# Kernel tuning notes

Measured on AMD Instinct MI355X. Metric: run time of the kernel, lower is better.

Reference implementation:

```python
import jax, jax.numpy as jnp
import numpy as np

RESO = 64
PAD = 0.1
SCALE = 8.0
PLANES = {'xz': (0, 2), 'xy': (0, 1), 'yz': (1, 2)}
PLANE_ORDER = ['xz', 'xy', 'yz']


def normalize_coordinate(p, plane):
    i, j = PLANES[plane]
    xy = jnp.stack([p[..., i], p[..., j]], axis=-1)
    xy = xy / (1.0 + PAD + 1e-3) + 0.5
    return jnp.clip(xy, 0.0, 1.0 - 1e-5)


def coordinate2index(xy, reso):
    x = (xy * reso).astype(jnp.int32)
    return x[..., 0] + reso * x[..., 1]  # (B, T)


def resblock(x, W0, b0, W1, b1, Ws):
    # ResnetBlockFC: fc_1(relu(fc_0(relu(x)))) + shortcut(x)
    net = jnp.maximum(x, 0.0) @ W0 + b0
    dx = jnp.maximum(net, 0.0) @ W1 + b1
    return x @ Ws + dx


def scatter_max_pool(c, idx_flat, num_seg):
    # c: (B, T, h); idx_flat: (B*T,) batch-offset plane indices
    B, T, h = c.shape
    pooled = jax.ops.segment_max(c.reshape(B * T, h), idx_flat, num_segments=num_seg)
    return pooled[idx_flat].reshape(B, T, h)


def plane_feature(p, c, plane):
    # scatter_mean of c into (B, c_dim, RESO, RESO); empty cells -> 0
    B, T, cd = c.shape
    R2 = RESO * RESO
    idx = coordinate2index(normalize_coordinate(p / SCALE, plane), RESO)
    idxf = (idx + jnp.arange(B, dtype=jnp.int32)[:, None] * R2).reshape(-1)
    sums = jax.ops.segment_sum(c.reshape(B * T, cd), idxf, num_segments=B * R2)
    cnt = jax.ops.segment_sum(jnp.ones((B * T,), c.dtype), idxf, num_segments=B * R2)
    mean = sums / jnp.maximum(cnt, 1.0)[:, None]
    return mean.reshape(B, R2, cd).transpose(0, 2, 1).reshape(B, cd, RESO, RESO)


def forward(p, fc_pos_W, fc_pos_b, blocks_W0, blocks_b0, blocks_W1, blocks_b1, blocks_Ws, fc_c_W, fc_c_b):
    B, T, _ = p.shape
    R2 = RESO * RESO
    offs = jnp.arange(B, dtype=jnp.int32)[:, None] * R2
    idx = {k: (coordinate2index(normalize_coordinate(p / SCALE, k), RESO) + offs).reshape(-1)
           for k in PLANE_ORDER}

    net = p @ fc_pos_W + fc_pos_b  # (B, T, 3h)
    net = resblock(net, blocks_W0[0], blocks_b0[0], blocks_W1[0], blocks_b1[0], blocks_Ws[0])
    n_blocks = blocks_W0.shape[0]
    for i in range(1, n_blocks):
        pooled = sum(scatter_max_pool(net, idx[k], B * R2) for k in PLANE_ORDER)
        meanp = jnp.broadcast_to(net.mean(axis=1, keepdims=True), net.shape)
        net = jnp.concatenate([net, pooled, meanp], axis=-1)  # (B, T, 3h)
        net = resblock(net, blocks_W0[i], blocks_b0[i], blocks_W1[i], blocks_b1[i], blocks_Ws[i])

    c = net @ fc_c_W + fc_c_b  # (B, T, c_dim)
    fea = jnp.stack([plane_feature(p, c, k) for k in PLANE_ORDER], axis=0)
    return fea  # (3, B, c_dim, RESO, RESO) in order xz, xy, yz


def setup_inputs() -> dict:
    key = jax.random.key(0)
    ks = jax.random.split(key, 10)
    B, T, dim = 16, 8192, 3
    h, c_dim, nb = 128, 128, 5
    s = 0.05
    return {
        'p': jax.random.normal(ks[0], (B, T, dim), jnp.float32) * 2.0,
        'fc_pos_W': jax.random.normal(ks[1], (dim, 3 * h), jnp.float32) * s,
        'fc_pos_b': jnp.zeros((3 * h,), jnp.float32),
        'blocks_W0': jax.random.normal(ks[2], (nb, 3 * h, h), jnp.float32) * s,
        'blocks_b0': jnp.zeros((nb, h), jnp.float32),
        'blocks_W1': jax.random.normal(ks[3], (nb, h, h), jnp.float32) * s,
        'blocks_b1': jnp.zeros((nb, h), jnp.float32),
        'blocks_Ws': jax.random.normal(ks[4], (nb, 3 * h, h), jnp.float32) * s,
        'fc_c_W': jax.random.normal(ks[5], (h, c_dim), jnp.float32) * s,
        'fc_c_b': jnp.zeros((c_dim,), jnp.float32),
    }


def reference(p, fc_pos_W, fc_pos_b, blocks_W0, blocks_b0, blocks_W1, blocks_b1, blocks_Ws, fc_c_W, fc_c_b):
    return forward(p, fc_pos_W, fc_pos_b, blocks_W0, blocks_b0, blocks_W1, blocks_b1, blocks_Ws, fc_c_W, fc_c_b)
```

## Files before the change

### kernel.cpp

```cpp
#include <hip/hip_runtime.h>

#define BT (16 * 8192)
#define NB 5
#define NCELL 65536
typedef unsigned int uint;
typedef unsigned short ushort;
typedef __attribute__((ext_vector_type(8))) short bf16x8;
typedef __attribute__((ext_vector_type(4))) float f32x4;


__device__ __forceinline__ uint f2bf(float x) {
    uint u = __float_as_uint(x);
    return (u + 0x7fffu + ((u >> 16) & 1u)) >> 16;
}
__device__ __forceinline__ float bf2f_lo(uint u) { return __uint_as_float(u << 16); }
__device__ __forceinline__ float bf2f_hi(uint u) { return __uint_as_float(u & 0xffff0000u); }
__device__ __forceinline__ uint pack2(float a, float b) { return f2bf(a) | (f2bf(b) << 16); }

__device__ __forceinline__ uint relu2(uint u) {
    uint m = (u >> 15) & 0x00010001u;
    return u & ~(m * 0xffffu);
}
__device__ __forceinline__ bf16x8 relu8(bf16x8 a) {
    uint4 u = *(uint4*)&a;
    u.x = relu2(u.x); u.y = relu2(u.y); u.z = relu2(u.z); u.w = relu2(u.w);
    return *(bf16x8*)&u;
}
__device__ __forceinline__ f32x4 bcast4(float x) { return (f32x4){x, x, x, x}; }
__device__ __forceinline__ f32x4 mfma16(bf16x8 a, bf16x8 b, f32x4 c) {
    return __builtin_amdgcn_mfma_f32_16x16x32_bf16(a, b, c, 0, 0, 0);
}

__global__ void k_idx(const float* __restrict__ p, int* __restrict__ idx) {
    int r = blockIdx.x * 256 + threadIdx.x;
    if (r >= BT) return;
    float p0 = p[3 * r + 0], p1 = p[3 * r + 1], p2 = p[3 * r + 2];
    const float DEN = (float)(1.0 + 0.1 + 1e-3);
    const float HI  = (float)(1.0 - 1e-5);
    int b = r >> 13;
    float x0 = fminf(fmaxf((p0 / 8.0f) / DEN + 0.5f, 0.0f), HI);
    float x1 = fminf(fmaxf((p1 / 8.0f) / DEN + 0.5f, 0.0f), HI);
    float x2 = fminf(fmaxf((p2 / 8.0f) / DEN + 0.5f, 0.0f), HI);
    int i0 = (int)(x0 * 64.0f);
    int i1 = (int)(x1 * 64.0f);
    int i2 = (int)(x2 * 64.0f);
    int base = b << 12;
    idx[r]          = base + i0 + (i2 << 6);
    idx[BT + r]     = base + i0 + (i1 << 6);
    idx[2 * BT + r] = base + i1 + (i2 << 6);
}

__global__ void k_hist(const int* __restrict__ idx, int* __restrict__ cnt) {
    int r = blockIdx.x * 256 + threadIdx.x;
    if (r >= BT) return;
    atomicAdd(cnt + idx[r], 1);
    atomicAdd(cnt + NCELL + idx[BT + r], 1);
    atomicAdd(cnt + 2 * NCELL + idx[2 * BT + r], 1);
}

__global__ __launch_bounds__(1024) void k_scan(const int* __restrict__ cnt,
                                               int* __restrict__ starts,
                                               int* __restrict__ cursor) {
    __shared__ int sc[1024];
    int pl = blockIdx.x, t = threadIdx.x;
    const int* c = cnt + pl * NCELL;
    int base = t * 64;
    int s = 0;
    for (int i = 0; i < 64; ++i) s += c[base + i];
    sc[t] = s;
    __syncthreads();
    for (int off = 1; off < 1024; off <<= 1) {
        int v = (t >= off) ? sc[t - off] : 0;
        __syncthreads();
        sc[t] += v;
        __syncthreads();
    }
    int run = sc[t] - s;
    for (int i = 0; i < 64; ++i) {
        int cell = base + i;
        starts[pl * NCELL + cell] = run;
        cursor[pl * NCELL + cell] = run;
        run += c[cell];
    }
}

__global__ void k_scatter_order(const int* __restrict__ idx, int* __restrict__ cursor,
                                int* __restrict__ order) {
    int r = blockIdx.x * 256 + threadIdx.x;
    if (r >= BT) return;
    for (int pl = 0; pl < 3; ++pl) {
        int cell = idx[pl * BT + r];
        int pos = atomicAdd(cursor + pl * NCELL + cell, 1);
        order[pl * BT + pos] = r;
    }
}

__global__ void k_wconv(const float* __restrict__ W0, const float* __restrict__ W1,
                        const float* __restrict__ Ws, const float* __restrict__ Wc,
                        ushort* __restrict__ wb) {
    int mat = blockIdx.y;
    int K = (mat < 5 || (mat >= 10 && mat < 15)) ? 384 : 128;
    int e = blockIdx.x * 256 + threadIdx.x;
    if (e >= K * 128) return;
    const float* src;
    size_t doff;
    if (mat < 5)       { src = W0 + (size_t)mat * 49152;        doff = (size_t)mat * 49152; }
    else if (mat < 10) { src = W1 + (size_t)(mat - 5) * 16384;  doff = 245760 + (size_t)(mat - 5) * 16384; }
    else if (mat < 15) { src = Ws + (size_t)(mat - 10) * 49152; doff = 327680 + (size_t)(mat - 10) * 49152; }
    else               { src = Wc;                              doff = 573440; }
    int ko = e & 31, n = (e >> 5) & 127, kt = e >> 12;
    wb[doff + e] = (ushort)f2bf(src[(size_t)(kt * 32 + ko) * 128 + n]);
}

__global__ __launch_bounds__(256) void k_segmax(const uint* __restrict__ netu,
                                                const int* __restrict__ starts,
                                                const int* __restrict__ cnt,
                                                const int* __restrict__ order,
                                                uint* __restrict__ segu) {
    int g = blockIdx.x * 4 + (threadIdx.x >> 6);
    int l = threadIdx.x & 63;
    int n = cnt[g];
    if (n == 0) return;
    int pl = g >> 16;
    const int* ord = order + pl * BT + starts[g];
    float m0 = -INFINITY, m1 = -INFINITY;
    int i = 0;
    for (; i + 4 <= n; i += 4) {
        uint a = netu[(size_t)ord[i] * 64 + l];
        uint b = netu[(size_t)ord[i + 1] * 64 + l];
        uint c = netu[(size_t)ord[i + 2] * 64 + l];
        uint d = netu[(size_t)ord[i + 3] * 64 + l];
        m0 = fmaxf(fmaxf(m0, fmaxf(bf2f_lo(a), bf2f_lo(b))), fmaxf(bf2f_lo(c), bf2f_lo(d)));
        m1 = fmaxf(fmaxf(m1, fmaxf(bf2f_hi(a), bf2f_hi(b))), fmaxf(bf2f_hi(c), bf2f_hi(d)));
    }
    for (; i < n; ++i) {
        uint a = netu[(size_t)ord[i] * 64 + l];
        m0 = fmaxf(m0, bf2f_lo(a));
        m1 = fmaxf(m1, bf2f_hi(a));
    }
    segu[(size_t)g * 64 + l] = pack2(m0, m1);
}

template <int MODE>
__global__ __launch_bounds__(512, 4) void k_resblock(
    const float* __restrict__ p, const uint* __restrict__ netu,
    const int* __restrict__ idxg, const ushort* __restrict__ seg,
    const float* __restrict__ meanR, const float* __restrict__ Wp,
    const float* __restrict__ bp, const ushort* __restrict__ wb0,
    const float* __restrict__ b0v, const ushort* __restrict__ wb1,
    const float* __restrict__ b1v, const ushort* __restrict__ wbs,
    ushort* __restrict__ out, float* __restrict__ meanW) {
    __shared__ __align__(16) ushort aT[64 * 392];
    __shared__ __align__(16) ushort hT[64 * 136];
    const int t = threadIdx.x;
    const int rowBase = blockIdx.x * 64;
    const int bb = rowBase >> 13;

    if constexpr (MODE == 0) {
        for (int f = t; f < 3072; f += 512) {
            int row = f / 48, g = f - row * 48;
            const float* pr = p + (size_t)(rowBase + row) * 3;
            float p0 = pr[0], p1 = pr[1], p2 = pr[2];
            int k0 = g * 8;
            uint d[4];
#pragma unroll
            for (int w = 0; w < 4; ++w) {
                int k = k0 + 2 * w;
                float v0 = bp[k]     + p0 * Wp[k]     + p1 * Wp[384 + k]     + p2 * Wp[768 + k];
                float v1 = bp[k + 1] + p0 * Wp[k + 1] + p1 * Wp[384 + k + 1] + p2 * Wp[768 + k + 1];
                d[w] = pack2(v0, v1);
            }
            *(uint4*)(aT + row * 392 + k0) = make_uint4(d[0], d[1], d[2], d[3]);
        }
    } else {
        const uint4* nsrc = (const uint4*)netu;
#pragma unroll
        for (int i = 0; i < 2; ++i) {
            int f = t + 512 * i;
            int row = f >> 4, cu = f & 15;
            *(uint4*)(aT + row * 392 + cu * 8) = nsrc[(size_t)(rowBase + row) * 16 + cu];
        }
#pragma unroll
        for (int i = 0; i < 2; ++i) {
            int f = t + 512 * i;
            int row = f >> 4, grp = f & 15;
            int prow = rowBase + row;
            float o[8] = {};
#pragma unroll
            for (int pl = 0; pl < 3; ++pl) {
                int cell = idxg[pl * BT + prow];
                uint4 s4 = *(const uint4*)(seg + (size_t)(pl * NCELL + cell) * 128 + grp * 8);
                o[0] += bf2f_lo(s4.x); o[1] += bf2f_hi(s4.x);
                o[2] += bf2f_lo(s4.y); o[3] += bf2f_hi(s4.y);
                o[4] += bf2f_lo(s4.z); o[5] += bf2f_hi(s4.z);
                o[6] += bf2f_lo(s4.w); o[7] += bf2f_hi(s4.w);
            }
            uint4 d = make_uint4(pack2(o[0], o[1]), pack2(o[2], o[3]),
                                 pack2(o[4], o[5]), pack2(o[6], o[7]));
            *(uint4*)(aT + row * 392 + 128 + grp * 8) = d;
        }
        {
            int grp = t & 15, rr = t >> 4;
            const float* ms = meanR + bb * 128 + grp * 8;
            uint4 d = make_uint4(pack2(ms[0], ms[1]), pack2(ms[2], ms[3]),
                                 pack2(ms[4], ms[5]), pack2(ms[6], ms[7]));
#pragma unroll
            for (int ii = 0; ii < 2; ++ii) {
                int row = rr + 32 * ii;
                *(uint4*)(aT + row * 392 + 256 + grp * 8) = d;
            }
        }
    }
    __syncthreads();

    const int l = t & 63, wid = t >> 6;
    const int n0 = wid * 16;
    const int lm = l & 15, lg = l >> 4;
    const ushort* w0 = wb0 + n0 * 32;
    const ushort* w1 = wb1 + n0 * 32;
    const ushort* ws = wbs + n0 * 32;

    f32x4 acc0[4], accS[4];
    {
        float bi = b0v[n0 + lm];
        float si = b1v[n0 + lm];
#pragma unroll
        for (int im = 0; im < 4; ++im) { acc0[im] = bcast4(bi); accS[im] = bcast4(si); }
    }
#pragma unroll
    for (int kt = 0; kt < 12; ++kt) {
        bf16x8 b0 = *(const bf16x8*)(w0 + kt * 4096 + lm * 32 + lg * 8);
        bf16x8 bs = *(const bf16x8*)(ws + kt * 4096 + lm * 32 + lg * 8);
#pragma unroll
        for (int im = 0; im < 4; ++im) {
            bf16x8 a = *(const bf16x8*)(aT + (im * 16 + lm) * 392 + kt * 32 + lg * 8);
            acc0[im] = mfma16(relu8(a), b0, acc0[im]);
            accS[im] = mfma16(a, bs, accS[im]);
        }
    }
#pragma unroll
    for (int im = 0; im < 4; ++im)
#pragma unroll
        for (int j = 0; j < 4; ++j) {
            int row = im * 16 + lg * 4 + j;
            hT[row * 136 + n0 + lm] = (ushort)f2bf(fmaxf(acc0[im][j], 0.0f));
        }
    __syncthreads();

#pragma unroll
    for (int kt = 0; kt < 4; ++kt) {
        bf16x8 b = *(const bf16x8*)(w1 + kt * 4096 + lm * 32 + lg * 8);
#pragma unroll
        for (int im = 0; im < 4; ++im) {
            bf16x8 a = *(const bf16x8*)(hT + (im * 16 + lm) * 136 + kt * 32 + lg * 8);
            accS[im] = mfma16(a, b, accS[im]);
        }
    }

#pragma unroll
    for (int im = 0; im < 4; ++im)
#pragma unroll
        for (int j = 0; j < 4; ++j) {
            int row = rowBase + im * 16 + lg * 4 + j;
            out[(size_t)row * 128 + n0 + lm] = (ushort)f2bf(accS[im][j]);
        }

    {
        float s = 0.0f;
#pragma unroll
        for (int im = 0; im < 4; ++im)
#pragma unroll
            for (int j = 0; j < 4; ++j) s += accS[im][j];
        s += __shfl_xor(s, 16);
        s += __shfl_xor(s, 32);
        if (l < 16) atomicAdd(meanW + bb * 128 + n0 + l, s * (1.0f / 8192.0f));
    }
}

__device__ __forceinline__ void mfma_gemm3(const ushort* __restrict__ aLDS, int lda, int nk,
                                           const ushort* __restrict__ wb, int lm, int lg,
                                           f32x4 acc[4][2]) {
    for (int kt = 0; kt < nk; ++kt) {
        bf16x8 b0 = *(const bf16x8*)(wb + kt * 4096 + lm * 32 + lg * 8);
        bf16x8 b1 = *(const bf16x8*)(wb + kt * 4096 + (16 + lm) * 32 + lg * 8);
#pragma unroll
        for (int im = 0; im < 4; ++im) {
            bf16x8 a = *(const bf16x8*)(aLDS + (im * 16 + lm) * lda + kt * 32 + lg * 8);
            acc[im][0] = mfma16(a, b0, acc[im][0]);
            acc[im][1] = mfma16(a, b1, acc[im][1]);
        }
    }
}

__global__ __launch_bounds__(256, 2) void k_fcc(const uint* __restrict__ netu,
                                                const ushort* __restrict__ wbc,
                                                const float* __restrict__ bc,
                                                ushort* __restrict__ cout) {
    __shared__ __align__(16) ushort aT[64 * 136];
    const int t = threadIdx.x;
    const int rowBase = blockIdx.x * 64;
    const uint4* nsrc = (const uint4*)netu;
#pragma unroll
    for (int i = 0; i < 4; ++i) {
        int u = t + 256 * i;
        int row = u >> 4, cu = u & 15;
        *(uint4*)(aT + row * 136 + cu * 8) = nsrc[(size_t)(rowBase + row) * 16 + cu];
    }
    __syncthreads();
    const int l = t & 63, wid = t >> 6;
    const int n0 = wid * 32;
    const int lm = l & 15, lg = l >> 4;
    f32x4 acc[4][2];
    {
        float ci0 = bc[n0 + lm], ci1 = bc[n0 + 16 + lm];
#pragma unroll
        for (int im = 0; im < 4; ++im) { acc[im][0] = bcast4(ci0); acc[im][1] = bcast4(ci1); }
    }
    mfma_gemm3(aT, 136, 4, wbc + n0 * 32, lm, lg, acc);
#pragma unroll
    for (int im = 0; im < 4; ++im)
#pragma unroll
        for (int ic = 0; ic < 2; ++ic)
#pragma unroll
            for (int j = 0; j < 4; ++j) {
                int row = rowBase + im * 16 + lg * 4 + j;
                int col = n0 + ic * 16 + lm;
                cout[(size_t)row * 128 + col] = (ushort)f2bf(acc[im][ic][j]);
            }
}

__global__ __launch_bounds__(256) void k_segsum(const uint* __restrict__ cp,
                                                const int* __restrict__ starts,
                                                const int* __restrict__ cnt,
                                                const int* __restrict__ order,
                                                float* __restrict__ sums, int pl) {
    int cell = blockIdx.x * 4 + (threadIdx.x >> 6);
    int l = threadIdx.x & 63;
    int n = cnt[pl * NCELL + cell];
    if (n == 0) return;
    const int* ord = order + pl * BT + starts[pl * NCELL + cell];
    float s0 = 0.f, s1 = 0.f;
    int i = 0;
    for (; i + 4 <= n; i += 4) {
        uint a = cp[(size_t)ord[i] * 64 + l];
        uint b = cp[(size_t)ord[i + 1] * 64 + l];
        uint c = cp[(size_t)ord[i + 2] * 64 + l];
        uint d = cp[(size_t)ord[i + 3] * 64 + l];
        s0 += (bf2f_lo(a) + bf2f_lo(b)) + (bf2f_lo(c) + bf2f_lo(d));
        s1 += (bf2f_hi(a) + bf2f_hi(b)) + (bf2f_hi(c) + bf2f_hi(d));
    }
    for (; i < n; ++i) {
        uint a = cp[(size_t)ord[i] * 64 + l];
        s0 += bf2f_lo(a);
        s1 += bf2f_hi(a);
    }
    *(float2*)(sums + (size_t)cell * 128 + 2 * l) = make_float2(s0, s1);
}

__global__ __launch_bounds__(256) void k_fin(const float* __restrict__ sums,
                                             const int* __restrict__ cnt,
                                             float* __restrict__ out, int pl) {
    __shared__ float tile[32][33];
    int t = threadIdx.x;
    int tx = t & 31, ty = t >> 5;
    int cl0 = (blockIdx.x & 127) << 5;
    int ch0 = (blockIdx.x >> 7) << 5;
    int b = blockIdx.y;
    int bc = b << 12;
#pragma unroll
    for (int j = 0; j < 4; ++j)
        tile[ty + 8 * j][tx] = sums[(size_t)(bc + cl0 + ty + 8 * j) * 128 + ch0 + tx];
    __syncthreads();
#pragma unroll
    for (int j = 0; j < 4; ++j) {
        int ch = ch0 + ty + 8 * j;
        int cl = cl0 + tx;
        int cn = cnt[pl * NCELL + bc + cl];
        float v = cn > 0 ? tile[tx][ty + 8 * j] / (float)cn : 0.0f;
        out[((size_t)((pl * 16 + b) * 128 + ch) << 12) + cl] = v;
    }
}

extern "C" void kernel_launch(void* const* d_in, const int* in_sizes, int n_in,
                              void* d_out, int out_size, void* d_ws, size_t ws_size,
                              hipStream_t stream) {
    const float* p  = (const float*)d_in[0];
    const float* Wp = (const float*)d_in[1];
    const float* bp = (const float*)d_in[2];
    const float* W0 = (const float*)d_in[3];
    const float* b0 = (const float*)d_in[4];
    const float* W1 = (const float*)d_in[5];
    const float* b1 = (const float*)d_in[6];
    const float* Ws = (const float*)d_in[7];
    const float* Wc = (const float*)d_in[8];
    const float* bc = (const float*)d_in[9];
    float* out = (float*)d_out;

    ushort* net    = (ushort*)d_ws;
    ushort* seg    = net + 16777216;
    float*  sums   = (float*)seg;
    ushort* wb     = seg + 25165824;
    int*    idx    = (int*)(wb + 589824);
    int*    order  = idx + 393216;
    int*    cnt    = order + 393216;
    int*    starts = cnt + 196608;
    int*    cursor = starts + 196608;
    float*  meanB  = (float*)(cursor + 196608);

    k_idx<<<512, 256, 0, stream>>>(p, idx);
    hipMemsetAsync(cnt, 0, 3 * NCELL * 4, stream);
    k_hist<<<512, 256, 0, stream>>>(idx, cnt);
    k_scan<<<3, 1024, 0, stream>>>(cnt, starts, cursor);
    k_scatter_order<<<512, 256, 0, stream>>>(idx, cursor, order);
    k_wconv<<<dim3(192, 16), 256, 0, stream>>>(W0, W1, Ws, Wc, wb);

    hipMemsetAsync(meanB, 0, 2048 * 4, stream);
    k_resblock<0><<<2048, 512, 0, stream>>>(
        p, nullptr, nullptr, nullptr, nullptr, Wp, bp,
        wb, b0, wb + 245760, b1, wb + 327680, net, meanB);

    for (int i = 1; i < NB; ++i) {
        k_segmax<<<49152, 256, 0, stream>>>((const uint*)net, starts, cnt, order, (uint*)seg);
        hipMemsetAsync(meanB + (i & 1) * 2048, 0, 2048 * 4, stream);
        k_resblock<1><<<2048, 512, 0, stream>>>(
            nullptr, (const uint*)net, idx, seg, meanB + ((i - 1) & 1) * 2048,
            nullptr, nullptr,
            wb + (size_t)i * 49152, b0 + i * 128,
            wb + 245760 + (size_t)i * 16384, b1 + i * 128,
            wb + 327680 + (size_t)i * 49152,
            net, meanB + (i & 1) * 2048);
    }

    k_fcc<<<2048, 256, 0, stream>>>((const uint*)net, wb + 573440, bc, net);

    for (int pl = 0; pl < 3; ++pl) {
        k_segsum<<<16384, 256, 0, stream>>>((const uint*)net, starts, cnt, order, sums, pl);
        k_fin<<<dim3(512, 16), 256, 0, stream>>>(sums, cnt, out, pl);
    }
}
```

Measured before the change: 769.1 us.

## Fold per-batch mean columns into a precomputed bias vector for resblocks

The mean-pooled third of each resblock input is constant across a batch, so its contribution through W0 (after relu) and Ws is now computed once per batch by a small kernel and used as the accumulator init. This shrinks the K dimension of the main GEMM from 384 to 256 and the shared A tile, which allows a higher occupancy hint in launch bounds. The last block skips the mean reduction, and the segmax/segsum tail loops are unrolled into predicated loads. The cost is an extra small kernel launch per block, and the bias now keeps the mean in fp32 rather than rounding it to bf16.

```diff
diff --git a/kernel.cpp b/kernel.cpp
--- a/kernel.cpp
+++ b/kernel.cpp
@@ -110,6 +110,31 @@
     else               { src = Wc;                              doff = 573440; }
     int ko = e & 31, n = (e >> 5) & 127, kt = e >> 12;
     wb[doff + e] = (ushort)f2bf(src[(size_t)(kt * 32 + ko) * 128 + n]);
+}
+
+__global__ __launch_bounds__(128) void k_meanvec(const float* __restrict__ meanB,
+                                                 const ushort* __restrict__ wb0,
+                                                 const float* __restrict__ b0v,
+                                                 const ushort* __restrict__ wbs,
+                                                 const float* __restrict__ b1v,
+                                                 float* __restrict__ rv0,
+                                                 float* __restrict__ rvS) {
+    __shared__ float ms[128];
+    int b = blockIdx.x, n = threadIdx.x;
+    ms[n] = meanB[b * 128 + n];
+    __syncthreads();
+    float s0 = b0v[n], ss = b1v[n];
+#pragma unroll 4
+    for (int k = 0; k < 128; ++k) {
+        float mv = ms[k];
+        int kt = 8 + (k >> 5), ko = k & 31;
+        float w0 = bf2f_lo((uint)wb0[kt * 4096 + n * 32 + ko]);
+        float ws = bf2f_lo((uint)wbs[kt * 4096 + n * 32 + ko]);
+        s0 = fmaf(fmaxf(mv, 0.0f), w0, s0);
+        ss = fmaf(mv, ws, ss);
+    }
+    rv0[b * 128 + n] = s0;
+    rvS[b * 128 + n] = ss;
 }
 
 __global__ __launch_bounds__(256) void k_segmax(const uint* __restrict__ netu,
@@ -133,24 +158,30 @@
         m0 = fmaxf(fmaxf(m0, fmaxf(bf2f_lo(a), bf2f_lo(b))), fmaxf(bf2f_lo(c), bf2f_lo(d)));
         m1 = fmaxf(fmaxf(m1, fmaxf(bf2f_hi(a), bf2f_hi(b))), fmaxf(bf2f_hi(c), bf2f_hi(d)));
     }
-    for (; i < n; ++i) {
+    int rem = n - i;
+    if (rem > 0) {
         uint a = netu[(size_t)ord[i] * 64 + l];
-        m0 = fmaxf(m0, bf2f_lo(a));
-        m1 = fmaxf(m1, bf2f_hi(a));
+        uint b = (rem > 1) ? netu[(size_t)ord[i + 1] * 64 + l] : a;
+        uint c = (rem > 2) ? netu[(size_t)ord[i + 2] * 64 + l] : a;
+        m0 = fmaxf(m0, fmaxf(bf2f_lo(a), fmaxf(bf2f_lo(b), bf2f_lo(c))));
+        m1 = fmaxf(m1, fmaxf(bf2f_hi(a), fmaxf(bf2f_hi(b), bf2f_hi(c))));
     }
     segu[(size_t)g * 64 + l] = pack2(m0, m1);
 }
 
 template <int MODE>
-__global__ __launch_bounds__(512, 4) void k_resblock(
+__global__ __launch_bounds__(512, 6) void k_resblock(
     const float* __restrict__ p, const uint* __restrict__ netu,
     const int* __restrict__ idxg, const ushort* __restrict__ seg,
-    const float* __restrict__ meanR, const float* __restrict__ Wp,
-    const float* __restrict__ bp, const ushort* __restrict__ wb0,
-    const float* __restrict__ b0v, const ushort* __restrict__ wb1,
-    const float* __restrict__ b1v, const ushort* __restrict__ wbs,
+    const float* __restrict__ rv0, const float* __restrict__ rvS,
+    const float* __restrict__ Wp, const float* __restrict__ bp,
+    const ushort* __restrict__ wb0, const float* __restrict__ b0v,
+    const ushort* __restrict__ wb1, const float* __restrict__ b1v,
+    const ushort* __restrict__ wbs,
     ushort* __restrict__ out, float* __restrict__ meanW) {
-    __shared__ __align__(16) ushort aT[64 * 392];
+    constexpr int LDA = (MODE == 0) ? 392 : 264;
+    constexpr int NKT = (MODE == 0) ? 12 : 8;
+    __shared__ __align__(16) ushort aT[64 * LDA];
     __shared__ __align__(16) ushort hT[64 * 136];
     const int t = threadIdx.x;
     const int rowBase = blockIdx.x * 64;
@@ -170,7 +201,7 @@
                 float v1 = bp[k + 1] + p0 * Wp[k + 1] + p1 * Wp[384 + k + 1] + p2 * Wp[768 + k + 1];
                 d[w] = pack2(v0, v1);
             }
-            *(uint4*)(aT + row * 392 + k0) = make_uint4(d[0], d[1], d[2], d[3]);
+            *(uint4*)(aT + row * LDA + k0) = make_uint4(d[0], d[1], d[2], d[3]);
         }
     } else {
         const uint4* nsrc = (const uint4*)netu;
@@ -178,7 +209,7 @@
         for (int i = 0; i < 2; ++i) {
             int f = t + 512 * i;
             int row = f >> 4, cu = f & 15;
-            *(uint4*)(aT + row * 392 + cu * 8) = nsrc[(size_t)(rowBase + row) * 16 + cu];
+            *(uint4*)(aT + row * LDA + cu * 8) = nsrc[(size_t)(rowBase + row) * 16 + cu];
         }
 #pragma unroll
         for (int i = 0; i < 2; ++i) {
@@ -197,18 +228,7 @@
             }
             uint4 d = make_uint4(pack2(o[0], o[1]), pack2(o[2], o[3]),
                                  pack2(o[4], o[5]), pack2(o[6], o[7]));
-            *(uint4*)(aT + row * 392 + 128 + grp * 8) = d;
-        }
-        {
-            int grp = t & 15, rr = t >> 4;
-            const float* ms = meanR + bb * 128 + grp * 8;
-            uint4 d = make_uint4(pack2(ms[0], ms[1]), pack2(ms[2], ms[3]),
-                                 pack2(ms[4], ms[5]), pack2(ms[6], ms[7]));
-#pragma unroll
-            for (int ii = 0; ii < 2; ++ii) {
-                int row = rr + 32 * ii;
-                *(uint4*)(aT + row * 392 + 256 + grp * 8) = d;
-            }
+            *(uint4*)(aT + row * LDA + 128 + grp * 8) = d;
         }
     }
     __syncthreads();
@@ -222,18 +242,19 @@
 
     f32x4 acc0[4], accS[4];
     {
-        float bi = b0v[n0 + lm];
-        float si = b1v[n0 + lm];
+        float bi, si;
+        if constexpr (MODE == 0) { bi = b0v[n0 + lm];            si = b1v[n0 + lm]; }
+        else                     { bi = rv0[bb * 128 + n0 + lm]; si = rvS[bb * 128 + n0 + lm]; }
 #pragma unroll
         for (int im = 0; im < 4; ++im) { acc0[im] = bcast4(bi); accS[im] = bcast4(si); }
     }
 #pragma unroll
-    for (int kt = 0; kt < 12; ++kt) {
+    for (int kt = 0; kt < NKT; ++kt) {
         bf16x8 b0 = *(const bf16x8*)(w0 + kt * 4096 + lm * 32 + lg * 8);
         bf16x8 bs = *(const bf16x8*)(ws + kt * 4096 + lm * 32 + lg * 8);
 #pragma unroll
         for (int im = 0; im < 4; ++im) {
-            bf16x8 a = *(const bf16x8*)(aT + (im * 16 + lm) * 392 + kt * 32 + lg * 8);
+            bf16x8 a = *(const bf16x8*)(aT + (im * 16 + lm) * LDA + kt * 32 + lg * 8);
             acc0[im] = mfma16(relu8(a), b0, acc0[im]);
             accS[im] = mfma16(a, bs, accS[im]);
         }
@@ -265,7 +286,7 @@
             out[(size_t)row * 128 + n0 + lm] = (ushort)f2bf(accS[im][j]);
         }
 
-    {
+    if (meanW) {
         float s = 0.0f;
 #pragma unroll
         for (int im = 0; im < 4; ++im)
@@ -349,10 +370,13 @@
         s0 += (bf2f_lo(a) + bf2f_lo(b)) + (bf2f_lo(c) + bf2f_lo(d));
         s1 += (bf2f_hi(a) + bf2f_hi(b)) + (bf2f_hi(c) + bf2f_hi(d));
     }
-    for (; i < n; ++i) {
+    int rem = n - i;
+    if (rem > 0) {
         uint a = cp[(size_t)ord[i] * 64 + l];
-        s0 += bf2f_lo(a);
-        s1 += bf2f_hi(a);
+        uint b = (rem > 1) ? cp[(size_t)ord[i + 1] * 64 + l] : 0u;
+        uint c = (rem > 2) ? cp[(size_t)ord[i + 2] * 64 + l] : 0u;
+        s0 += bf2f_lo(a) + (bf2f_lo(b) + bf2f_lo(c));
+        s1 += bf2f_hi(a) + (bf2f_hi(b) + bf2f_hi(c));
     }
     *(float2*)(sums + (size_t)cell * 128 + 2 * l) = make_float2(s0, s1);
 }
@@ -406,6 +430,8 @@
     int*    starts = cnt + 196608;
     int*    cursor = starts + 196608;
     float*  meanB  = (float*)(cursor + 196608);
+    float*  rv0    = meanB + 2 * 2048;
+    float*  rvS    = rv0 + 2048;
 
     k_idx<<<512, 256, 0, stream>>>(p, idx);
     hipMemsetAsync(cnt, 0, 3 * NCELL * 4, stream);
@@ -416,19 +442,24 @@
 
     hipMemsetAsync(meanB, 0, 2048 * 4, stream);
     k_resblock<0><<<2048, 512, 0, stream>>>(
-        p, nullptr, nullptr, nullptr, nullptr, Wp, bp,
+        p, nullptr, nullptr, nullptr, nullptr, nullptr, Wp, bp,
         wb, b0, wb + 245760, b1, wb + 327680, net, meanB);
 
     for (int i = 1; i < NB; ++i) {
+        const ushort* wb0i = wb + (size_t)i * 49152;
+        const ushort* wb1i = wb + 245760 + (size_t)i * 16384;
+        const ushort* wbsi = wb + 327680 + (size_t)i * 49152;
         k_segmax<<<49152, 256, 0, stream>>>((const uint*)net, starts, cnt, order, (uint*)seg);
-        hipMemsetAsync(meanB + (i & 1) * 2048, 0, 2048 * 4, stream);
+        k_meanvec<<<16, 128, 0, stream>>>(meanB + ((i - 1) & 1) * 2048,
+                                          wb0i, b0 + i * 128, wbsi, b1 + i * 128, rv0, rvS);
+        float* mw = nullptr;
+        if (i < NB - 1) {
+            mw = meanB + (i & 1) * 2048;
+            hipMemsetAsync(mw, 0, 2048 * 4, stream);
+        }
         k_resblock<1><<<2048, 512, 0, stream>>>(
-            nullptr, (const uint*)net, idx, seg, meanB + ((i - 1) & 1) * 2048,
-            nullptr, nullptr,
-            wb + (size_t)i * 49152, b0 + i * 128,
-            wb + 245760 + (size_t)i * 16384, b1 + i * 128,
-            wb + 327680 + (size_t)i * 49152,
-            net, meanB + (i & 1) * 2048);
+            nullptr, (const uint*)net, idx, seg, rv0, rvS, nullptr, nullptr,
+            wb0i, nullptr, wb1i, nullptr, wbsi, net, mw);
     }
 
     k_fcc<<<2048, 256, 0, stream>>>((const uint*)net, wb + 573440, bc, net);
```

Result: no change. 765.1 us (-0.5%).
